# Kernel optimization log

Hardware: AMD Instinct MI355X
Metric: run time of the kernel (lower is better)

Reference implementation:

```python
import jax, jax.numpy as jnp
import numpy as np

EPS = 1e-5
# NOTE: TransmorpherLayer2d passes (dim_head, num_heads) into TiedAxialSelfAttention2d(num_heads, dim_head),
# so with init dim_head=64, num_heads=8 the attention effectively uses H=64 heads of C=8 channels each.
H = 64
C = 8


def _ln_ch(x, w, b):
    # AxialLayerNorm over channel dim (dim=1) of [B, D, S, L]
    m = x.mean(axis=1, keepdims=True)
    v = x.var(axis=1, keepdims=True)
    return (x - m) * jax.lax.rsqrt(v + EPS) * w[None, :, None, None] + b[None, :, None, None]


def _conv1x1(x, W, b):
    # Conv2d kernel_size=1: pointwise channel mix. W: [out, in], x: [B, in, S, L]
    return jnp.einsum('od,bdsl->bosl', W, x) + b[None, :, None, None]


def setup_inputs() -> dict:
    key = jax.random.key(0)
    ks = jax.random.split(key, 8)
    B, D, S, L, F = 1, 512, 64, 256, 2048
    g = lambda k, shape: jax.random.normal(k, shape, jnp.float32) * 0.02
    return {
        'x': jax.random.normal(ks[0], (B, D, S, L), jnp.float32),
        'w_row': g(ks[1], (3 * D, D)), 'b_row': jnp.zeros((3 * D,), jnp.float32),
        'w_col': g(ks[2], (3 * D, D)), 'b_col': jnp.zeros((3 * D,), jnp.float32),
        'w_an1': jnp.ones((D,), jnp.float32), 'b_an1': jnp.zeros((D,), jnp.float32),
        'w_an2': jnp.ones((D,), jnp.float32), 'b_an2': jnp.zeros((D,), jnp.float32),
        'w_ff1': g(ks[3], (F, D)), 'b_ff1': jnp.zeros((F,), jnp.float32),
        'w_ff2': g(ks[4], (D, F)), 'b_ff2': jnp.zeros((D,), jnp.float32),
        'w_ln1': jnp.ones((D,), jnp.float32), 'b_ln1': jnp.zeros((D,), jnp.float32),
        'w_ln2': jnp.ones((D,), jnp.float32), 'b_ln2': jnp.zeros((D,), jnp.float32),
    }


def _forward(x, w_row, b_row, w_col, b_col, w_an1, b_an1, w_an2, b_an2,
             w_ff1, b_ff1, w_ff2, b_ff2, w_ln1, b_ln1, w_ln2, b_ln2):
    B, D, S, L = x.shape
    # ---- tied row attention (attention tied across the S axis; no 1/sqrt scaling in source) ----
    qkv = _conv1x1(x, w_row, b_row)
    q, k, v = [t.reshape(B, H, C, S, L) for t in jnp.split(qkv, 3, axis=1)]
    row_attn = jax.nn.softmax(jnp.einsum('bhcsi,bhcsj->bhij', q, k), axis=-1)  # [B,H,L,L]
    row_out = jnp.einsum('bhij,bhdsj->bhdsi', row_attn, v).reshape(B, D, S, L)
    out = _ln_ch(x + row_out, w_an1, b_an1)
    # ---- column attention (softmax over key index j = dim -2) ----
    qkv = _conv1x1(out, w_col, b_col)
    q, k, v = [t.reshape(B, H, C, S, L) for t in jnp.split(qkv, 3, axis=1)]
    col_attn = jax.nn.softmax(jnp.einsum('bhcil,bhcjl->bhijl', q, k), axis=-2)  # [B,H,S,S,L]
    col_out = jnp.einsum('bhijl,bhdjl->bhdil', col_attn, v).reshape(B, D, S, L)
    attn_out = _ln_ch(out + col_out, w_an2, b_an2)
    # ---- layer body. Source bug kept faithfully: the attention residual `x + dropout1(out)`
    # is computed then discarded; norm1 is applied to the attention output only. ----
    h = _ln_ch(attn_out, w_ln1, b_ln1)
    ff = _conv1x1(jax.nn.relu(_conv1x1(h, w_ff1, b_ff1)), w_ff2, b_ff2)
    return _ln_ch(h + ff, w_ln2, b_ln2)


def reference(x, w_row, b_row, w_col, b_col, w_an1, b_an1, w_an2, b_an2,
              w_ff1, b_ff1, w_ff2, b_ff2, w_ln1, b_ln1, w_ln2, b_ln2):
    return _forward(x, w_row, b_row, w_col, b_col, w_an1, b_an1, w_an2, b_an2,
                    w_ff1, b_ff1, w_ff2, b_ff2, w_ln1, b_ln1, w_ln2, b_ln2)
```

## Files before the change

kernel.cpp:

```cpp
#include <hip/hip_runtime.h>
#include <hip/hip_bf16.h>

using s16x8 = __attribute__((ext_vector_type(8))) short;
using f32x4 = __attribute__((ext_vector_type(4))) float;
using u32x2 = __attribute__((ext_vector_type(2))) unsigned;

__device__ __forceinline__ ushort f2bf(float f) {
  union { float f; unsigned u; } v; v.f = f;
  unsigned r = v.u + 0x7fffu + ((v.u >> 16) & 1u);
  return (ushort)(r >> 16);
}
__device__ __forceinline__ float bf2f(ushort u) {
  return __uint_as_float(((unsigned)u) << 16);
}
__device__ __forceinline__ void gload16(const void* g, void* l) {
  __builtin_amdgcn_global_load_lds(
      (const __attribute__((address_space(1))) void*)g,
      (__attribute__((address_space(3))) void*)l, 16, 0, 0);
}

template<int AF, int BF, bool BIAS, bool RELU, int OUT, bool TRC>
__global__ __launch_bounds__(256, 3)
void gemm(void* __restrict__ Cv, const ushort* __restrict__ A,
          const ushort* __restrict__ B, const float* __restrict__ bias,
          int K, int lda, int ldb, int ldc, long sA, long sB, long sC)
{
  __shared__ ushort As[2][5120];
  __shared__ ushort Bs[2][5120];
  const int tid  = threadIdx.x;
  const int lane = tid & 63, wid = tid >> 6;
  const int gx = gridDim.x, gy = gridDim.y;
  const int lin = blockIdx.y * gx + blockIdx.x;
  int mb, nb;
  if ((gx & 7) == 0) {
    const int xcd = lin & 7, idx = lin >> 3, gxp = gx >> 3;
    nb = xcd * gxp + idx / gy;
    mb = idx % gy;
  } else {
    const int nwg = gx * gy;
    const int swz = ((nwg & 7) == 0) ? ((lin & 7) * (nwg >> 3) + (lin >> 3)) : lin;
    mb = swz / gx; nb = swz % gx;
  }
  const int m0 = mb * 128, n0 = nb * 128;
  A += (long)blockIdx.z * sA;
  B += (long)blockIdx.z * sB;

  const int wm = (wid >> 1) * 64, wn = (wid & 1) * 64;
  const int fr = lane & 15, kg = lane >> 4;

  f32x4 acc[4][4];
#pragma unroll
  for (int i = 0; i < 4; ++i)
#pragma unroll
    for (int j = 0; j < 4; ++j)
#pragma unroll
      for (int r = 0; r < 4; ++r) acc[i][j][r] = 0.f;

  auto stageT = [&](const ushort* __restrict__ G, int ld, int c0,
                    ushort* lds, int k0) {
#pragma unroll
    for (int c = 0; c < 2; ++c) {
      const int nb2 = wid * 2 + c;
      const ushort* gp = G + (long)(k0 + (lane >> 1)) * ld + c0 + nb2 * 16 + (lane & 1) * 8;
      gload16(gp, lds + nb2 * 512);
    }
  };
  auto loadN = [&](const ushort* __restrict__ G, int ld, int r0, int k0,
                   uint4& x, uint4& y) {
    const ushort* gp = G + (long)(r0 + (tid >> 1)) * ld + k0 + (tid & 1) * 8;
    x = *(const uint4*)gp;
    y = *(const uint4*)(gp + 16);
  };
  auto writeN = [&](ushort* lds, uint4 x, uint4 y) {
    ushort* p = lds + (tid >> 1) * 40 + (tid & 1) * 8;
    *(uint4*)p = x;
    *(uint4*)(p + 16) = y;
  };
  auto fragN = [&](const ushort* lds, int row) {
    union { s16x8 f; u32x2 h[2]; } u;
    const ushort* p = lds + row * 40 + kg * 4;
    u.h[0] = *(const u32x2*)p;
    u.h[1] = *(const u32x2*)(p + 16);
    return u.f;
  };
  auto fragT = [&](const ushort* lds, int rb) {
    union { s16x8 f; u32x2 h[2]; } u;
    unsigned base = (unsigned)(unsigned long long)(lds + rb * 512) + lane * 8;
    asm volatile("ds_read_b64_tr_b16 %0, %1" : "=v"(u.h[0]) : "v"(base));
    asm volatile("ds_read_b64_tr_b16 %0, %1 offset:512" : "=v"(u.h[1]) : "v"(base));
    return u.f;
  };

  const int NT = K >> 5;
  uint4 ax, ay, bx, by;

  if constexpr (AF == 0) { loadN(A, lda, m0, 0, ax, ay); writeN(As[0], ax, ay); }
  else                   { stageT(A, lda, m0, As[0], 0); }
  if constexpr (BF == 0) { loadN(B, ldb, n0, 0, bx, by); writeN(Bs[0], bx, by); }
  else                   { stageT(B, ldb, n0, Bs[0], 0); }
  __syncthreads();

  for (int t = 0; t < NT; ++t) {
    const int cur = t & 1, nxt = cur ^ 1;
    const bool pre = (t + 1) < NT;
    if (pre) {
      if constexpr (AF == 0) loadN(A, lda, m0, (t + 1) << 5, ax, ay);
      else                   stageT(A, lda, m0, As[nxt], (t + 1) << 5);
      if constexpr (BF == 0) loadN(B, ldb, n0, (t + 1) << 5, bx, by);
      else                   stageT(B, ldb, n0, Bs[nxt], (t + 1) << 5);
    }
    s16x8 af[4], bv[4];
#pragma unroll
    for (int m = 0; m < 4; ++m) {
      if constexpr (AF == 0) af[m] = fragN(As[cur], wm + m * 16 + fr);
      else                   af[m] = fragT(As[cur], (wm >> 4) + m);
    }
#pragma unroll
    for (int n = 0; n < 4; ++n) {
      if constexpr (BF == 0) bv[n] = fragN(Bs[cur], wn + n * 16 + fr);
      else                   bv[n] = fragT(Bs[cur], (wn >> 4) + n);
    }
    if constexpr (AF == 1 || BF == 1) {
      asm volatile("s_waitcnt lgkmcnt(0)");
      __builtin_amdgcn_sched_barrier(0);
    }
    __builtin_amdgcn_s_setprio(1);
#pragma unroll
    for (int m = 0; m < 4; ++m)
#pragma unroll
      for (int n = 0; n < 4; ++n)
        acc[m][n] = __builtin_amdgcn_mfma_f32_16x16x32_bf16(af[m], bv[n], acc[m][n], 0, 0, 0);
    __builtin_amdgcn_s_setprio(0);
    if (pre) {
      if constexpr (AF == 0) writeN(As[nxt], ax, ay);
      if constexpr (BF == 0) writeN(Bs[nxt], bx, by);
    }
    __syncthreads();
  }

#pragma unroll
  for (int m = 0; m < 4; ++m) {
    const int rowb = m0 + wm + m * 16 + kg * 4;
#pragma unroll
    for (int n = 0; n < 4; ++n) {
      const int col = n0 + wn + n * 16 + fr;
      f32x4 v = acc[m][n];
      if constexpr (BIAS) {
#pragma unroll
        for (int r = 0; r < 4; ++r) v[r] += bias[rowb + r];
      }
      if constexpr (RELU) {
#pragma unroll
        for (int r = 0; r < 4; ++r) v[r] = fmaxf(v[r], 0.f);
      }
      if constexpr (TRC) {
        if constexpr (OUT == 0) {
          float* C = (float*)Cv + (long)blockIdx.z * sC;
          float4 s; s.x = v[0]; s.y = v[1]; s.z = v[2]; s.w = v[3];
          *(float4*)(C + (long)col * ldc + rowb) = s;
        } else {
          ushort* C = (ushort*)Cv + (long)blockIdx.z * sC;
          ushort4 s; s.x = f2bf(v[0]); s.y = f2bf(v[1]); s.z = f2bf(v[2]); s.w = f2bf(v[3]);
          *(ushort4*)(C + (long)col * ldc + rowb) = s;
        }
      } else if constexpr (OUT == 0) {
        float* C = (float*)Cv + (long)blockIdx.z * sC;
#pragma unroll
        for (int r = 0; r < 4; ++r) C[(long)(rowb + r) * ldc + col] = v[r];
      } else {
        ushort* C = (ushort*)Cv + (long)blockIdx.z * sC;
#pragma unroll
        for (int r = 0; r < 4; ++r) C[(long)(rowb + r) * ldc + col] = f2bf(v[r]);
      }
    }
  }
}

__global__ __launch_bounds__(256)
void cvt_kernel(const float4* __restrict__ in, ushort4* __restrict__ out, int n4) {
  int i = blockIdx.x * 256 + threadIdx.x;
  if (i < n4) {
    float4 f = in[i];
    ushort4 u; u.x = f2bf(f.x); u.y = f2bf(f.y); u.z = f2bf(f.z); u.w = f2bf(f.w);
    out[i] = u;
  }
}

__global__ __launch_bounds__(256)
void softmax_kernel(const float* __restrict__ S, ushort* __restrict__ P) {
  const int row = blockIdx.x * 4 + (threadIdx.x >> 6);
  const int lane = threadIdx.x & 63;
  float4 v = *(const float4*)(S + (long)row * 256 + lane * 4);
  float mx = fmaxf(fmaxf(v.x, v.y), fmaxf(v.z, v.w));
#pragma unroll
  for (int off = 32; off; off >>= 1) mx = fmaxf(mx, __shfl_xor(mx, off));
  v.x = __expf(v.x - mx); v.y = __expf(v.y - mx);
  v.z = __expf(v.z - mx); v.w = __expf(v.w - mx);
  float s = v.x + v.y + v.z + v.w;
#pragma unroll
  for (int off = 32; off; off >>= 1) s += __shfl_xor(s, off);
  const float r = 1.f / s;
  ushort4 o;
  o.x = f2bf(v.x * r); o.y = f2bf(v.y * r); o.z = f2bf(v.z * r); o.w = f2bf(v.w * r);
  *(ushort4*)(P + (long)row * 256 + lane * 4) = o;
}

__global__ __launch_bounds__(256)
void colattn_kernel(const ushort* __restrict__ qkv, ushort* __restrict__ out) {
  __shared__ float q[4][8][64], kk[4][8][64], vv[4][8][64];
  const int lin = blockIdx.x;
  const int swz = (lin & 7) * 512 + (lin >> 3);
  const int h = swz >> 6;
  const int l0 = (swz & 63) * 4;
  const int tid = threadIdx.x;
  for (int i = tid; i < 1536; i += 256) {
    int m = i >> 9;
    int e = i & 511;
    int c = e >> 6, s = e & 63;
    ushort4 u = *(const ushort4*)(qkv + (long)(m * 512 + h * 8 + c) * 16384 + s * 256 + l0);
    float* dst = (m == 0) ? &q[0][0][0] : (m == 1) ? &kk[0][0][0] : &vv[0][0][0];
    dst[e] = bf2f(u.x); dst[512 + e] = bf2f(u.y);
    dst[1024 + e] = bf2f(u.z); dst[1536 + e] = bf2f(u.w);
  }
  __syncthreads();
  const int li = tid >> 6, lane = tid & 63;
  float qi[8];
#pragma unroll
  for (int c = 0; c < 8; ++c) qi[c] = q[li][c][lane];
  float sc[64];
#pragma unroll
  for (int j4 = 0; j4 < 16; ++j4) {
    float ax = 0.f, ay = 0.f, az = 0.f, aw = 0.f;
#pragma unroll
    for (int c = 0; c < 8; ++c) {
      float4 k4 = *(const float4*)&kk[li][c][j4 * 4];
      ax = fmaf(qi[c], k4.x, ax); ay = fmaf(qi[c], k4.y, ay);
      az = fmaf(qi[c], k4.z, az); aw = fmaf(qi[c], k4.w, aw);
    }
    sc[j4 * 4 + 0] = ax; sc[j4 * 4 + 1] = ay;
    sc[j4 * 4 + 2] = az; sc[j4 * 4 + 3] = aw;
  }
  float mx = sc[0];
#pragma unroll
  for (int j = 1; j < 64; ++j) mx = fmaxf(mx, sc[j]);
  float sum = 0.f;
#pragma unroll
  for (int j = 0; j < 64; ++j) { sc[j] = __expf(sc[j] - mx); sum += sc[j]; }
  const float rs = 1.f / sum;
  float o[8];
#pragma unroll
  for (int c = 0; c < 8; ++c) o[c] = 0.f;
#pragma unroll
  for (int j4 = 0; j4 < 16; ++j4) {
    const float px = sc[j4 * 4 + 0], py = sc[j4 * 4 + 1];
    const float pz = sc[j4 * 4 + 2], pw = sc[j4 * 4 + 3];
#pragma unroll
    for (int c = 0; c < 8; ++c) {
      float4 v4 = *(const float4*)&vv[li][c][j4 * 4];
      o[c] = fmaf(px, v4.x, fmaf(py, v4.y, fmaf(pz, v4.z, fmaf(pw, v4.w, o[c]))));
    }
  }
#pragma unroll
  for (int c = 0; c < 8; ++c) q[li][c][lane] = o[c] * rs;
  __syncthreads();
  for (int i = tid; i < 512; i += 256) {
    int c = i >> 6, s = i & 63;
    ushort4 u;
    u.x = f2bf(q[0][c][s]); u.y = f2bf(q[1][c][s]);
    u.z = f2bf(q[2][c][s]); u.w = f2bf(q[3][c][s]);
    *(ushort4*)(out + (long)(h * 8 + c) * 16384 + s * 256 + l0) = u;
  }
}

template<bool RES, int OM>
__global__ __launch_bounds__(1024)
void ln_kernel(void* __restrict__ outv, const ushort* __restrict__ a,
               const ushort* __restrict__ b, const float* __restrict__ w,
               const float* __restrict__ bias) {
  __shared__ float red[2][16][64];
  const int lane = threadIdx.x & 63, seg = threadIdx.x >> 6;
  const long n = (long)blockIdx.x * 64 + lane;
  const int d0 = seg * 32;
  float v[32];
  float s1 = 0.f, s2 = 0.f;
#pragma unroll
  for (int i = 0; i < 32; ++i) {
    float t = bf2f(a[(long)(d0 + i) * 16384 + n]);
    if constexpr (RES) t += bf2f(b[(long)(d0 + i) * 16384 + n]);
    v[i] = t; s1 += t; s2 += t * t;
  }
  red[0][seg][lane] = s1; red[1][seg][lane] = s2;
  __syncthreads();
  s1 = 0.f; s2 = 0.f;
#pragma unroll
  for (int s = 0; s < 16; ++s) { s1 += red[0][s][lane]; s2 += red[1][s][lane]; }
  const float mean = s1 * (1.f / 512.f);
  const float var = s2 * (1.f / 512.f) - mean * mean;
  const float rstd = rsqrtf(var + 1e-5f);
#pragma unroll
  for (int i = 0; i < 32; ++i) {
    float o = (v[i] - mean) * rstd * w[d0 + i] + bias[d0 + i];
    if constexpr (OM == 0) ((ushort*)outv)[(long)(d0 + i) * 16384 + n] = f2bf(o);
    else                   ((float*)outv)[(long)(d0 + i) * 16384 + n] = o;
  }
}

__global__ __launch_bounds__(1024)
void ln_fuse_kernel(ushort* __restrict__ out, const ushort* __restrict__ a,
                    const ushort* __restrict__ b,
                    const float* __restrict__ w1, const float* __restrict__ b1,
                    const float* __restrict__ w2, const float* __restrict__ b2) {
  __shared__ float red[2][16][64];
  const int lane = threadIdx.x & 63, seg = threadIdx.x >> 6;
  const long n = (long)blockIdx.x * 64 + lane;
  const int d0 = seg * 32;
  float v[32];
  float s1 = 0.f, s2 = 0.f;
#pragma unroll
  for (int i = 0; i < 32; ++i) {
    float t = bf2f(a[(long)(d0 + i) * 16384 + n]) + bf2f(b[(long)(d0 + i) * 16384 + n]);
    v[i] = t; s1 += t; s2 += t * t;
  }
  red[0][seg][lane] = s1; red[1][seg][lane] = s2;
  __syncthreads();
  s1 = 0.f; s2 = 0.f;
#pragma unroll
  for (int s = 0; s < 16; ++s) { s1 += red[0][s][lane]; s2 += red[1][s][lane]; }
  float mean = s1 * (1.f / 512.f);
  float var = s2 * (1.f / 512.f) - mean * mean;
  float rstd = rsqrtf(var + 1e-5f);
  __syncthreads();
  s1 = 0.f; s2 = 0.f;
#pragma unroll
  for (int i = 0; i < 32; ++i) {
    float y = (v[i] - mean) * rstd * w1[d0 + i] + b1[d0 + i];
    v[i] = y; s1 += y; s2 += y * y;
  }
  red[0][seg][lane] = s1; red[1][seg][lane] = s2;
  __syncthreads();
  s1 = 0.f; s2 = 0.f;
#pragma unroll
  for (int s = 0; s < 16; ++s) { s1 += red[0][s][lane]; s2 += red[1][s][lane]; }
  mean = s1 * (1.f / 512.f);
  var = s2 * (1.f / 512.f) - mean * mean;
  rstd = rsqrtf(var + 1e-5f);
#pragma unroll
  for (int i = 0; i < 32; ++i) {
    float o = (v[i] - mean) * rstd * w2[d0 + i] + b2[d0 + i];
    out[(long)(d0 + i) * 16384 + n] = f2bf(o);
  }
}

extern "C" void kernel_launch(void* const* d_in, const int* in_sizes, int n_in,
                              void* d_out, int out_size, void* d_ws, size_t ws_size,
                              hipStream_t stream) {
  const float* x     = (const float*)d_in[0];
  const float* w_row = (const float*)d_in[1];
  const float* b_row = (const float*)d_in[2];
  const float* w_col = (const float*)d_in[3];
  const float* b_col = (const float*)d_in[4];
  const float* w_an1 = (const float*)d_in[5];
  const float* b_an1 = (const float*)d_in[6];
  const float* w_an2 = (const float*)d_in[7];
  const float* b_an2 = (const float*)d_in[8];
  const float* w_ff1 = (const float*)d_in[9];
  const float* b_ff1 = (const float*)d_in[10];
  const float* w_ff2 = (const float*)d_in[11];
  const float* b_ff2 = (const float*)d_in[12];
  const float* w_ln1 = (const float*)d_in[13];
  const float* b_ln1 = (const float*)d_in[14];
  const float* w_ln2 = (const float*)d_in[15];
  const float* b_ln2 = (const float*)d_in[16];
  float* outp = (float*)d_out;

  char* Wb = (char*)d_ws;
  ushort* big    = (ushort*)Wb;
  float*  sc     = (float*)(Wb + 71303168ull);
  ushort* colbf  = (ushort*)(Wb + 71303168ull);
  ushort* P      = (ushort*)(Wb + 90177536ull);
  ushort* xbf    = (ushort*)(Wb + 100663296ull);
  ushort* ff2bf  = (ushort*)(Wb + 100663296ull);
  ushort* rowbf  = (ushort*)(Wb + 118489088ull);
  ushort* out1bf = (ushort*)(Wb + 136314880ull);
  ushort* hbf    = (ushort*)(Wb + 154140672ull);
  ushort* wrowb  = (ushort*)(Wb + 171966464ull);
  ushort* wcolb = wrowb + 786432;
  ushort* wff1b = wcolb + 786432;
  ushort* wff2b = wff1b + 1048576;

  const dim3 blk(256);
  const long HQ = 131072;
  const long HS = 65536;

  cvt_kernel<<<8192, blk, 0, stream>>>((const float4*)x, (ushort4*)xbf, 2097152);
  cvt_kernel<<<768,  blk, 0, stream>>>((const float4*)w_row, (ushort4*)wrowb, 196608);
  cvt_kernel<<<768,  blk, 0, stream>>>((const float4*)w_col, (ushort4*)wcolb, 196608);
  cvt_kernel<<<1024, blk, 0, stream>>>((const float4*)w_ff1, (ushort4*)wff1b, 262144);
  cvt_kernel<<<1024, blk, 0, stream>>>((const float4*)w_ff2, (ushort4*)wff2b, 262144);

  gemm<0,1,true,false,1,false><<<dim3(128, 12, 1), blk, 0, stream>>>(
      big, wrowb, xbf, b_row, 512, 512, 16384, 16384, 0, 0, 0);
  gemm<1,1,false,false,0,false><<<dim3(2, 2, 64), blk, 0, stream>>>(
      sc, big, big + (long)512 * 16384, nullptr, 512, 256, 256, 256, HQ, HQ, HS);
  softmax_kernel<<<4096, blk, 0, stream>>>(sc, P);
  gemm<0,0,false,false,1,true><<<dim3(4, 2, 64), blk, 0, stream>>>(
      rowbf, P, big + (long)1024 * 16384, nullptr, 256, 256, 256, 256, HS, HQ, HQ);
  ln_kernel<true, 0><<<256, dim3(1024), 0, stream>>>(out1bf, xbf, rowbf, w_an1, b_an1);
  gemm<0,1,true,false,1,false><<<dim3(128, 12, 1), blk, 0, stream>>>(
      big, wcolb, out1bf, b_col, 512, 512, 16384, 16384, 0, 0, 0);
  colattn_kernel<<<4096, blk, 0, stream>>>(big, colbf);
  ln_fuse_kernel<<<256, dim3(1024), 0, stream>>>(hbf, out1bf, colbf,
                                                 w_an2, b_an2, w_ln1, b_ln1);
  gemm<0,1,true,true,1,false><<<dim3(128, 16, 1), blk, 0, stream>>>(
      big, wff1b, hbf, b_ff1, 512, 512, 16384, 16384, 0, 0, 0);
  gemm<0,1,true,false,1,false><<<dim3(128, 4, 1), blk, 0, stream>>>(
      ff2bf, wff2b, big, b_ff2, 2048, 2048, 16384, 16384, 0, 0, 0);
  ln_kernel<true, 1><<<256, dim3(1024), 0, stream>>>(outp, hbf, ff2bf, w_ln2, b_ln2);
}
```

Before: 433.7 us.

## Fuse row attention QK, softmax and PV into one kernel

Replaces the three launches for tied row attention (score GEMM, softmax kernel, PV GEMM) with a single kernel per (head, 64-query block). Scores stay in LDS as fp32, softmax runs there, and the bf16 probabilities feed MFMA directly against double-buffered V tiles. This removes the global round trip of the fp32 score and bf16 probability matrices and two launches. In exchange it uses about 120KB of LDS per block, so only one block fits per CU, and the grid is just 256 blocks.

```diff
diff --git a/kernel.cpp b/kernel.cpp
--- a/kernel.cpp
+++ b/kernel.cpp
@@ -177,6 +177,187 @@
 }
 
 __global__ __launch_bounds__(256)
+void rowattn_kernel(const ushort* __restrict__ qkv, ushort* __restrict__ out) {
+  __shared__ __align__(16) char smem[122880];
+  ushort* stg = (ushort*)(smem + 81920);
+  float*  S   = (float*)smem;
+  ushort* P   = (ushort*)(smem + 81920);
+  ushort* Vs  = (ushort*)smem;
+
+  const int tid = threadIdx.x, lane = tid & 63, wid = tid >> 6;
+  const int fr = lane & 15, kg = lane >> 4;
+  const int lin = blockIdx.x;
+  const int swz = (lin & 7) * 32 + (lin >> 3);
+  const int h = swz >> 2, i0 = (swz & 3) * 64;
+  const ushort* Qh = qkv + (long)h * 131072;
+  const ushort* Kh = qkv + (long)512 * 16384 + (long)h * 131072;
+  const ushort* Vh = qkv + (long)1024 * 16384 + (long)h * 131072;
+
+  auto stage1 = [&](ushort* buf, int k0) {
+    for (int ch = wid; ch < 20; ch += 4) {
+      const ushort* G = (ch < 4) ? (Qh + i0 + ch * 16) : (Kh + (ch - 4) * 16);
+      gload16(G + (long)(k0 + (lane >> 1)) * 256 + (lane & 1) * 8, buf + ch * 512);
+    }
+  };
+  auto fragT = [&](const ushort* lds, int rb) {
+    union { s16x8 f; u32x2 h2[2]; } u;
+    unsigned base = (unsigned)(unsigned long long)(lds + rb * 512) + lane * 8;
+    asm volatile("ds_read_b64_tr_b16 %0, %1" : "=v"(u.h2[0]) : "v"(base));
+    asm volatile("ds_read_b64_tr_b16 %0, %1 offset:512" : "=v"(u.h2[1]) : "v"(base));
+    return u.f;
+  };
+
+  {
+    f32x4 acc[4][4];
+#pragma unroll
+    for (int m = 0; m < 4; ++m)
+#pragma unroll
+      for (int n = 0; n < 4; ++n)
+#pragma unroll
+        for (int r = 0; r < 4; ++r) acc[m][n][r] = 0.f;
+
+    stage1(stg, 0);
+    __syncthreads();
+    for (int t = 0; t < 16; ++t) {
+      ushort* cur = stg + (t & 1) * 10240;
+      ushort* nxt = stg + ((t & 1) ^ 1) * 10240;
+      if (t + 1 < 16) stage1(nxt, (t + 1) * 32);
+      s16x8 qf[4], kf[4];
+#pragma unroll
+      for (int m = 0; m < 4; ++m) qf[m] = fragT(cur, m);
+#pragma unroll
+      for (int n = 0; n < 4; ++n) kf[n] = fragT(cur, 4 + wid * 4 + n);
+      asm volatile("s_waitcnt lgkmcnt(0)");
+      __builtin_amdgcn_sched_barrier(0);
+      __builtin_amdgcn_s_setprio(1);
+#pragma unroll
+      for (int m = 0; m < 4; ++m)
+#pragma unroll
+        for (int n = 0; n < 4; ++n)
+          acc[m][n] = __builtin_amdgcn_mfma_f32_16x16x32_bf16(qf[m], kf[n], acc[m][n], 0, 0, 0);
+      __builtin_amdgcn_s_setprio(0);
+      __syncthreads();
+    }
+#pragma unroll
+    for (int m = 0; m < 4; ++m)
+#pragma unroll
+      for (int n = 0; n < 4; ++n)
+#pragma unroll
+        for (int r = 0; r < 4; ++r)
+          S[(m * 16 + kg * 4 + r) * 260 + wid * 64 + n * 16 + fr] = acc[m][n][r];
+  }
+  __syncthreads();
+
+  {
+    const int row = wid * 16 + (lane >> 2), p = lane & 3;
+    float* Sr = S + row * 260 + p * 64;
+    float mx = -3.4e38f;
+#pragma unroll
+    for (int t = 0; t < 16; ++t) {
+      float4 v = ((const float4*)Sr)[t];
+      mx = fmaxf(mx, fmaxf(fmaxf(v.x, v.y), fmaxf(v.z, v.w)));
+    }
+    mx = fmaxf(mx, __shfl_xor(mx, 1));
+    mx = fmaxf(mx, __shfl_xor(mx, 2));
+    float e[64];
+    float sum = 0.f;
+#pragma unroll
+    for (int t = 0; t < 16; ++t) {
+      float4 v = ((const float4*)Sr)[t];
+      e[4*t+0] = __expf(v.x - mx); e[4*t+1] = __expf(v.y - mx);
+      e[4*t+2] = __expf(v.z - mx); e[4*t+3] = __expf(v.w - mx);
+      sum += e[4*t+0] + e[4*t+1] + e[4*t+2] + e[4*t+3];
+    }
+    sum += __shfl_xor(sum, 1);
+    sum += __shfl_xor(sum, 2);
+    const float rs = 1.f / sum;
+    ushort* Pr = P + row * 260 + p * 64;
+#pragma unroll
+    for (int t = 0; t < 16; ++t) {
+      ushort4 o;
+      o.x = f2bf(e[4*t+0] * rs); o.y = f2bf(e[4*t+1] * rs);
+      o.z = f2bf(e[4*t+2] * rs); o.w = f2bf(e[4*t+3] * rs);
+      ((ushort4*)Pr)[t] = o;
+    }
+  }
+  __syncthreads();
+
+  {
+    f32x4 a2[8][4];
+#pragma unroll
+    for (int m = 0; m < 8; ++m)
+#pragma unroll
+      for (int n = 0; n < 4; ++n)
+#pragma unroll
+        for (int r = 0; r < 4; ++r) a2[m][n][r] = 0.f;
+
+    uint4 vx[4], vy[4];
+    auto vload = [&](int k0) {
+#pragma unroll
+      for (int rp = 0; rp < 4; ++rp) {
+        const ushort* gp = Vh + (long)(rp * 128 + (tid >> 1)) * 256 + k0 + (tid & 1) * 8;
+        vx[rp] = *(const uint4*)gp;
+        vy[rp] = *(const uint4*)(gp + 16);
+      }
+    };
+    auto vwrite = [&](ushort* buf) {
+#pragma unroll
+      for (int rp = 0; rp < 4; ++rp) {
+        ushort* p = buf + (rp * 128 + (tid >> 1)) * 40 + (tid & 1) * 8;
+        *(uint4*)p = vx[rp];
+        *(uint4*)(p + 16) = vy[rp];
+      }
+    };
+    vload(0); vwrite(Vs);
+    __syncthreads();
+    for (int t = 0; t < 8; ++t) {
+      ushort* cur = Vs + (t & 1) * 20480;
+      ushort* nxt = Vs + ((t & 1) ^ 1) * 20480;
+      const bool pre = (t + 1) < 8;
+      if (pre) vload((t + 1) * 32);
+      s16x8 vf[8], pf[4];
+#pragma unroll
+      for (int m = 0; m < 8; ++m) {
+        union { s16x8 f; u32x2 h2[2]; } u;
+        const ushort* p = cur + (wid * 128 + m * 16 + fr) * 40 + kg * 4;
+        u.h2[0] = *(const u32x2*)p;
+        u.h2[1] = *(const u32x2*)(p + 16);
+        vf[m] = u.f;
+      }
+#pragma unroll
+      for (int n = 0; n < 4; ++n) {
+        union { s16x8 f; u32x2 h2[2]; } u;
+        const ushort* p = P + (n * 16 + fr) * 260 + t * 32 + kg * 4;
+        u.h2[0] = *(const u32x2*)p;
+        u.h2[1] = *(const u32x2*)(p + 16);
+        pf[n] = u.f;
+      }
+      __builtin_amdgcn_s_setprio(1);
+#pragma unroll
+      for (int m = 0; m < 8; ++m)
+#pragma unroll
+        for (int n = 0; n < 4; ++n)
+          a2[m][n] = __builtin_amdgcn_mfma_f32_16x16x32_bf16(vf[m], pf[n], a2[m][n], 0, 0, 0);
+      __builtin_amdgcn_s_setprio(0);
+      if (pre) vwrite(nxt);
+      __syncthreads();
+    }
+    ushort* Oh = out + (long)h * 131072;
+#pragma unroll
+    for (int m = 0; m < 8; ++m) {
+      const int cs = wid * 128 + m * 16 + kg * 4;
+#pragma unroll
+      for (int n = 0; n < 4; ++n) {
+        const int i = i0 + n * 16 + fr;
+#pragma unroll
+        for (int r = 0; r < 4; ++r)
+          Oh[(long)(cs + r) * 256 + i] = f2bf(a2[m][n][r]);
+      }
+    }
+  }
+}
+
+__global__ __launch_bounds__(256)
 void cvt_kernel(const float4* __restrict__ in, ushort4* __restrict__ out, int n4) {
   int i = blockIdx.x * 256 + threadIdx.x;
   if (i < n4) {
@@ -184,25 +365,6 @@
     ushort4 u; u.x = f2bf(f.x); u.y = f2bf(f.y); u.z = f2bf(f.z); u.w = f2bf(f.w);
     out[i] = u;
   }
-}
-
-__global__ __launch_bounds__(256)
-void softmax_kernel(const float* __restrict__ S, ushort* __restrict__ P) {
-  const int row = blockIdx.x * 4 + (threadIdx.x >> 6);
-  const int lane = threadIdx.x & 63;
-  float4 v = *(const float4*)(S + (long)row * 256 + lane * 4);
-  float mx = fmaxf(fmaxf(v.x, v.y), fmaxf(v.z, v.w));
-#pragma unroll
-  for (int off = 32; off; off >>= 1) mx = fmaxf(mx, __shfl_xor(mx, off));
-  v.x = __expf(v.x - mx); v.y = __expf(v.y - mx);
-  v.z = __expf(v.z - mx); v.w = __expf(v.w - mx);
-  float s = v.x + v.y + v.z + v.w;
-#pragma unroll
-  for (int off = 32; off; off >>= 1) s += __shfl_xor(s, off);
-  const float r = 1.f / s;
-  ushort4 o;
-  o.x = f2bf(v.x * r); o.y = f2bf(v.y * r); o.z = f2bf(v.z * r); o.w = f2bf(v.w * r);
-  *(ushort4*)(P + (long)row * 256 + lane * 4) = o;
 }
 
 __global__ __launch_bounds__(256)
@@ -375,9 +537,7 @@
 
   char* Wb = (char*)d_ws;
   ushort* big    = (ushort*)Wb;
-  float*  sc     = (float*)(Wb + 71303168ull);
   ushort* colbf  = (ushort*)(Wb + 71303168ull);
-  ushort* P      = (ushort*)(Wb + 90177536ull);
   ushort* xbf    = (ushort*)(Wb + 100663296ull);
   ushort* ff2bf  = (ushort*)(Wb + 100663296ull);
   ushort* rowbf  = (ushort*)(Wb + 118489088ull);
@@ -389,8 +549,6 @@
   ushort* wff2b = wff1b + 1048576;
 
   const dim3 blk(256);
-  const long HQ = 131072;
-  const long HS = 65536;
 
   cvt_kernel<<<8192, blk, 0, stream>>>((const float4*)x, (ushort4*)xbf, 2097152);
   cvt_kernel<<<768,  blk, 0, stream>>>((const float4*)w_row, (ushort4*)wrowb, 196608);
@@ -400,11 +558,7 @@
 
   gemm<0,1,true,false,1,false><<<dim3(128, 12, 1), blk, 0, stream>>>(
       big, wrowb, xbf, b_row, 512, 512, 16384, 16384, 0, 0, 0);
-  gemm<1,1,false,false,0,false><<<dim3(2, 2, 64), blk, 0, stream>>>(
-      sc, big, big + (long)512 * 16384, nullptr, 512, 256, 256, 256, HQ, HQ, HS);
-  softmax_kernel<<<4096, blk, 0, stream>>>(sc, P);
-  gemm<0,0,false,false,1,true><<<dim3(4, 2, 64), blk, 0, stream>>>(
-      rowbf, P, big + (long)1024 * 16384, nullptr, 256, 256, 256, 256, HS, HQ, HQ);
+  rowattn_kernel<<<256, blk, 0, stream>>>(big, rowbf);
   ln_kernel<true, 0><<<256, dim3(1024), 0, stream>>>(out1bf, xbf, rowbf, w_an1, b_an1);
   gemm<0,1,true,false,1,false><<<dim3(128, 12, 1), blk, 0, stream>>>(
       big, wcolb, out1bf, b_col, 512, 512, 16384, 16384, 0, 0, 0);
```

After: 442.7 us. 2.1% more time.
